# Performance work log

Hardware: AMD Instinct MI355X
Metric: run time of the kernel (lower is better)

The kernel has to match this reference:

```python
import jax, jax.numpy as jnp
import numpy as np

FACTOR = 1.0

def _dct_matrix():
    n = 8
    D = np.zeros((n * n, n * n), dtype=np.float32)
    for u in range(n):
        for v in range(n):
            au = 1.0 / np.sqrt(2.0) if u == 0 else 1.0
            av = 1.0 / np.sqrt(2.0) if v == 0 else 1.0
            alpha = au * av * 0.25
            for x in range(n):
                for y in range(n):
                    D[u * n + v, x * n + y] = alpha * np.cos((2 * x + 1) * u * np.pi / 16) * np.cos((2 * y + 1) * v * np.pi / 16)
    return D

def _y_quant_table():
    t = np.array([[16, 11, 10, 16, 24, 40, 51, 61], [12, 12, 14, 19, 26, 58, 60, 55],
                  [14, 13, 16, 24, 40, 57, 69, 56], [14, 17, 22, 29, 51, 87, 80, 62],
                  [18, 22, 37, 56, 68, 109, 103, 77], [24, 35, 55, 64, 81, 104, 113, 92],
                  [49, 64, 78, 87, 103, 121, 120, 101], [72, 92, 95, 98, 112, 100, 103, 99]],
                 dtype=np.float32).T
    return t

def _c_quant_table():
    t = np.full((8, 8), 99, dtype=np.float32)
    t[:4, :4] = np.array([[17, 18, 24, 47], [18, 21, 26, 66], [24, 26, 56, 99], [47, 66, 99, 99]],
                          dtype=np.float32).T
    return t

_D = jnp.asarray(_dct_matrix())          # [64,64]
_QT = jnp.stack([jnp.asarray(_y_quant_table()),
                 jnp.asarray(_c_quant_table()),
                 jnp.asarray(_c_quant_table())], axis=0) * FACTOR  # [3,8,8]

def setup_inputs() -> dict:
    key = jax.random.key(0)
    image = jax.random.uniform(key, (32, 3, 512, 512), dtype=jnp.float32)
    return {"image": image}

def _diffjpeg(image):
    x = jnp.clip(image, 0.0, 1.0)
    B, C, H, W = x.shape  # H, W multiples of 8 -> no padding branch
    r, g, b = x[:, 0], x[:, 1], x[:, 2]
    y = 0.299 * r + 0.587 * g + 0.114 * b
    cb = (b - y) * 0.564 + 0.5
    cr = (r - y) * 0.713 + 0.5
    ycbcr = jnp.stack([y, cb, cr], axis=1)  # [B,3,H,W]
    # blockify into 8x8 tiles
    nh, nw = H // 8, W // 8
    blocks = ycbcr.reshape(B, C, nh, 8, nw, 8).transpose(0, 1, 2, 4, 3, 5)  # [B,C,nh,nw,8,8]
    flat = blocks.reshape(-1, 64) * 255.0 - 128.0
    dct = flat @ _D.T                      # matmul(D, flat.T).T
    dctb = dct.reshape(B, C, nh, nw, 8, 8)
    qte = _QT[None, :, None, None, :, :]   # [1,3,1,1,8,8]
    q = dctb / qte
    q = q + jax.lax.stop_gradient(jnp.round(q) - q)  # STE rounding
    deq = q * qte
    idct = deq.reshape(-1, 64) @ _D        # matmul(D.T, x.T).T
    idct = (idct + 128.0) / 255.0
    img = idct.reshape(B, C, nh, nw, 8, 8).transpose(0, 1, 2, 4, 3, 5).reshape(B, C, H, W)
    yy, ycb, ycr = img[:, 0], img[:, 1] - 0.5, img[:, 2] - 0.5
    rr = yy + 1.403 * ycr
    gg = yy - 0.714 * ycr - 0.344 * ycb
    bb = yy + 1.773 * ycb
    rgb = jnp.clip(jnp.stack([rr, gg, bb], axis=1), 0.0, 1.0)
    return jnp.clip(rgb, 0.0, 1.0)

def reference(image):
    return _diffjpeg(image)
```

## Files before the change

kernel.cpp:

```cpp
#include <hip/hip_runtime.h>

static constexpr float CM[8][8] = {
    { 0.353553391f,  0.353553391f,  0.353553391f,  0.353553391f,  0.353553391f,  0.353553391f,  0.353553391f,  0.353553391f},
    { 0.490392640f,  0.415734806f,  0.277785117f,  0.097545161f, -0.097545161f, -0.277785117f, -0.415734806f, -0.490392640f},
    { 0.461939766f,  0.191341716f, -0.191341716f, -0.461939766f, -0.461939766f, -0.191341716f,  0.191341716f,  0.461939766f},
    { 0.415734806f, -0.097545161f, -0.490392640f, -0.277785117f,  0.277785117f,  0.490392640f,  0.097545161f, -0.415734806f},
    { 0.353553391f, -0.353553391f, -0.353553391f,  0.353553391f,  0.353553391f, -0.353553391f, -0.353553391f,  0.353553391f},
    { 0.277785117f, -0.490392640f,  0.097545161f,  0.415734806f, -0.415734806f, -0.097545161f,  0.490392640f, -0.277785117f},
    { 0.191341716f, -0.461939766f,  0.461939766f, -0.191341716f, -0.191341716f,  0.461939766f, -0.461939766f,  0.191341716f},
    { 0.097545161f, -0.277785117f,  0.415734806f, -0.490392640f,  0.490392640f, -0.415734806f,  0.277785117f, -0.097545161f}
};

__device__ const float YQ[64] = {
    16.f, 11.f, 10.f, 16.f,  24.f,  40.f,  51.f,  61.f,
    12.f, 12.f, 14.f, 19.f,  26.f,  58.f,  60.f,  55.f,
    14.f, 13.f, 16.f, 24.f,  40.f,  57.f,  69.f,  56.f,
    14.f, 17.f, 22.f, 29.f,  51.f,  87.f,  80.f,  62.f,
    18.f, 22.f, 37.f, 56.f,  68.f, 109.f, 103.f,  77.f,
    24.f, 35.f, 55.f, 64.f,  81.f, 104.f, 113.f,  92.f,
    49.f, 64.f, 78.f, 87.f, 103.f, 121.f, 120.f, 101.f,
    72.f, 92.f, 95.f, 98.f, 112.f, 100.f, 103.f,  99.f
};

__device__ const float CQ[64] = {
    17.f, 18.f, 24.f, 47.f, 99.f, 99.f, 99.f, 99.f,
    18.f, 21.f, 26.f, 66.f, 99.f, 99.f, 99.f, 99.f,
    24.f, 26.f, 56.f, 99.f, 99.f, 99.f, 99.f, 99.f,
    47.f, 66.f, 99.f, 99.f, 99.f, 99.f, 99.f, 99.f,
    99.f, 99.f, 99.f, 99.f, 99.f, 99.f, 99.f, 99.f,
    99.f, 99.f, 99.f, 99.f, 99.f, 99.f, 99.f, 99.f,
    99.f, 99.f, 99.f, 99.f, 99.f, 99.f, 99.f, 99.f,
    99.f, 99.f, 99.f, 99.f, 99.f, 99.f, 99.f, 99.f
};

#define LDSW 68

__global__ __launch_bounds__(256, 6) void diffjpeg_kernel(const float* __restrict__ in,
                                                          float* __restrict__ out)
{
    __shared__ __align__(16) float pl[3][32][LDSW];

    const int t   = threadIdx.x;
    const int col = t & 63;
    const int br  = t >> 6;

    const int bid  = blockIdx.x;
    const int img  = bid >> 7;
    const int rem  = bid & 127;
    const int trow = rem >> 3;
    const int tcol = rem & 7;
    const size_t HW = (size_t)512 * 512;
    const size_t tbase = (size_t)img * 3 * HW + (size_t)(trow * 32) * 512 + (size_t)(tcol * 64);
    const float* __restrict__ pin  = in  + tbase;
    float* __restrict__       pout = out + tbase;

    {
        const float* cbase = pin + (size_t)(br * 8) * 512 + col;
        float rv[8], gv[8], bv[8];
        #pragma unroll
        for (int x = 0; x < 8; ++x) rv[x] = cbase[(size_t)x * 512];
        #pragma unroll
        for (int x = 0; x < 8; ++x) gv[x] = cbase[HW + (size_t)x * 512];
        #pragma unroll
        for (int x = 0; x < 8; ++x) bv[x] = cbase[2 * HW + (size_t)x * 512];

        float yv[8], cbv[8], crv[8];
        #pragma unroll
        for (int x = 0; x < 8; ++x) {
            const float r = fminf(fmaxf(rv[x], 0.f), 1.f);
            const float g = fminf(fmaxf(gv[x], 0.f), 1.f);
            const float b = fminf(fmaxf(bv[x], 0.f), 1.f);
            const float y  = 0.299f * r + 0.587f * g + 0.114f * b;
            yv[x]  = y * 255.f - 128.f;
            cbv[x] = ((b - y) * 0.564f + 0.5f) * 255.f - 128.f;
            crv[x] = ((r - y) * 0.713f + 0.5f) * 255.f - 128.f;
        }

        #pragma unroll
        for (int u = 0; u < 8; ++u) {
            float sy = 0.f, scb = 0.f, scr = 0.f;
            #pragma unroll
            for (int x = 0; x < 8; ++x) {
                sy  += CM[u][x] * yv[x];
                scb += CM[u][x] * cbv[x];
                scr += CM[u][x] * crv[x];
            }
            pl[0][br * 8 + u][col] = sy;
            pl[1][br * 8 + u][col] = scb;
            pl[2][br * 8 + u][col] = scr;
        }
    }
    __syncthreads();

    {
        const int bc  = t & 7;
        const int u   = (t >> 3) & 7;
        const int row = (t >> 6) * 8 + u;
        #pragma unroll
        for (int c = 0; c < 3; ++c) {
            float4* rp = (float4*)&pl[c][row][bc * 8];
            const float4 a0 = rp[0];
            const float4 a1 = rp[1];
            const float T[8] = {a0.x, a0.y, a0.z, a0.w, a1.x, a1.y, a1.z, a1.w};
            float Dq[8];
            #pragma unroll
            for (int v = 0; v < 8; ++v) {
                float s = 0.f;
                #pragma unroll
                for (int y = 0; y < 8; ++y) s += CM[v][y] * T[y];
                const float qt = (c == 0) ? YQ[v * 8 + u] : CQ[u * 8 + v];
                Dq[v] = rintf(s / qt) * qt;
            }
            float4 o0, o1;
            float* op = (float*)&o0;
            #pragma unroll
            for (int y = 0; y < 8; ++y) {
                float s = 0.f;
                #pragma unroll
                for (int v = 0; v < 8; ++v) s += Dq[v] * CM[v][y];
                if (y < 4) op[y] = s; else ((float*)&o1)[y - 4] = s;
            }
            rp[0] = o0;
            rp[1] = o1;
        }
    }
    __syncthreads();

    {
        float Xy[8], Xcb[8], Xcr[8];
        #pragma unroll
        for (int u = 0; u < 8; ++u) {
            Xy[u]  = pl[0][br * 8 + u][col];
            Xcb[u] = pl[1][br * 8 + u][col];
            Xcr[u] = pl[2][br * 8 + u][col];
        }
        float* obase = pout + (size_t)(br * 8) * 512 + col;
        constexpr float inv255 = 1.0f / 255.0f;
        #pragma unroll
        for (int x = 0; x < 8; ++x) {
            float sy = 0.f, scb = 0.f, scr = 0.f;
            #pragma unroll
            for (int u = 0; u < 8; ++u) {
                sy  += CM[u][x] * Xy[u];
                scb += CM[u][x] * Xcb[u];
                scr += CM[u][x] * Xcr[u];
            }
            const float yy = (sy  + 128.f) * inv255;
            const float cb = (scb + 128.f) * inv255 - 0.5f;
            const float cr = (scr + 128.f) * inv255 - 0.5f;
            const float rr = yy + 1.403f * cr;
            const float gg = yy - 0.714f * cr - 0.344f * cb;
            const float bb = yy + 1.773f * cb;
            obase[(size_t)x * 512]          = fminf(fmaxf(rr, 0.f), 1.f);
            obase[HW + (size_t)x * 512]     = fminf(fmaxf(gg, 0.f), 1.f);
            obase[2 * HW + (size_t)x * 512] = fminf(fmaxf(bb, 0.f), 1.f);
        }
    }
}

extern "C" void kernel_launch(void* const* d_in, const int* in_sizes, int n_in,
                              void* d_out, int out_size, void* d_ws, size_t ws_size,
                              hipStream_t stream) {
    const float* in = (const float*)d_in[0];
    float* out = (float*)d_out;
    const int B = in_sizes[0] / (3 * 512 * 512);
    const int grid = B * 128;
    diffjpeg_kernel<<<grid, 256, 0, stream>>>(in, out);
}
```

Before: 42.08 us.

## Use butterfly DCT, wave-local LDS fences, folded color constants, nontemporal stores

```diff
diff --git a/kernel.cpp b/kernel.cpp
--- a/kernel.cpp
+++ b/kernel.cpp
@@ -1,28 +1,25 @@
 #include <hip/hip_runtime.h>
 
-static constexpr float CM[8][8] = {
-    { 0.353553391f,  0.353553391f,  0.353553391f,  0.353553391f,  0.353553391f,  0.353553391f,  0.353553391f,  0.353553391f},
-    { 0.490392640f,  0.415734806f,  0.277785117f,  0.097545161f, -0.097545161f, -0.277785117f, -0.415734806f, -0.490392640f},
-    { 0.461939766f,  0.191341716f, -0.191341716f, -0.461939766f, -0.461939766f, -0.191341716f,  0.191341716f,  0.461939766f},
-    { 0.415734806f, -0.097545161f, -0.490392640f, -0.277785117f,  0.277785117f,  0.490392640f,  0.097545161f, -0.415734806f},
-    { 0.353553391f, -0.353553391f, -0.353553391f,  0.353553391f,  0.353553391f, -0.353553391f, -0.353553391f,  0.353553391f},
-    { 0.277785117f, -0.490392640f,  0.097545161f,  0.415734806f, -0.415734806f, -0.097545161f,  0.490392640f, -0.277785117f},
-    { 0.191341716f, -0.461939766f,  0.461939766f, -0.191341716f, -0.191341716f,  0.461939766f, -0.461939766f,  0.191341716f},
-    { 0.097545161f, -0.277785117f,  0.415734806f, -0.490392640f,  0.490392640f, -0.415734806f,  0.277785117f, -0.097545161f}
+#define K4 0.353553391f
+#define K1 0.490392640f
+#define K3 0.415734806f
+#define K5 0.277785117f
+#define K7 0.097545161f
+#define K2 0.461939766f
+#define K6 0.191341716f
+
+__device__ __align__(16) const float YQT[64] = {
+    16.f, 12.f, 14.f, 14.f,  18.f,  24.f,  49.f,  72.f,
+    11.f, 12.f, 13.f, 17.f,  22.f,  35.f,  64.f,  92.f,
+    10.f, 14.f, 16.f, 22.f,  37.f,  55.f,  78.f,  95.f,
+    16.f, 19.f, 24.f, 29.f,  56.f,  64.f,  87.f,  98.f,
+    24.f, 26.f, 40.f, 51.f,  68.f,  81.f, 103.f, 112.f,
+    40.f, 58.f, 57.f, 87.f, 109.f, 104.f, 121.f, 100.f,
+    51.f, 60.f, 69.f, 80.f, 103.f, 113.f, 120.f, 103.f,
+    61.f, 55.f, 56.f, 62.f,  77.f,  92.f, 101.f,  99.f
 };
 
-__device__ const float YQ[64] = {
-    16.f, 11.f, 10.f, 16.f,  24.f,  40.f,  51.f,  61.f,
-    12.f, 12.f, 14.f, 19.f,  26.f,  58.f,  60.f,  55.f,
-    14.f, 13.f, 16.f, 24.f,  40.f,  57.f,  69.f,  56.f,
-    14.f, 17.f, 22.f, 29.f,  51.f,  87.f,  80.f,  62.f,
-    18.f, 22.f, 37.f, 56.f,  68.f, 109.f, 103.f,  77.f,
-    24.f, 35.f, 55.f, 64.f,  81.f, 104.f, 113.f,  92.f,
-    49.f, 64.f, 78.f, 87.f, 103.f, 121.f, 120.f, 101.f,
-    72.f, 92.f, 95.f, 98.f, 112.f, 100.f, 103.f,  99.f
-};
-
-__device__ const float CQ[64] = {
+__device__ __align__(16) const float CQ[64] = {
     17.f, 18.f, 24.f, 47.f, 99.f, 99.f, 99.f, 99.f,
     18.f, 21.f, 26.f, 66.f, 99.f, 99.f, 99.f, 99.f,
     24.f, 26.f, 56.f, 99.f, 99.f, 99.f, 99.f, 99.f,
@@ -33,6 +30,41 @@
     99.f, 99.f, 99.f, 99.f, 99.f, 99.f, 99.f, 99.f
 };
 
+__device__ __forceinline__ void dct8(const float x[8], float X[8]) {
+    const float a0 = x[0] + x[7], a1 = x[1] + x[6], a2 = x[2] + x[5], a3 = x[3] + x[4];
+    const float d0 = x[0] - x[7], d1 = x[1] - x[6], d2 = x[2] - x[5], d3 = x[3] - x[4];
+    const float e0 = a0 + a3, e1 = a1 + a2, f0 = a0 - a3, f1 = a1 - a2;
+    X[0] = K4 * (e0 + e1);
+    X[4] = K4 * (e0 - e1);
+    X[2] = K2 * f0 + K6 * f1;
+    X[6] = K6 * f0 - K2 * f1;
+    X[1] = K1 * d0 + K3 * d1 + K5 * d2 + K7 * d3;
+    X[3] = K3 * d0 - K7 * d1 - K1 * d2 - K5 * d3;
+    X[5] = K5 * d0 - K1 * d1 + K7 * d2 + K3 * d3;
+    X[7] = K7 * d0 - K5 * d1 + K3 * d2 - K1 * d3;
+}
+
+__device__ __forceinline__ void idct8(const float X[8], float x[8]) {
+    const float g0 = K4 * (X[0] + X[4]);
+    const float g1 = K4 * (X[0] - X[4]);
+    const float E0 = g0 + K2 * X[2] + K6 * X[6];
+    const float E1 = g1 + K6 * X[2] - K2 * X[6];
+    const float E2 = g1 - K6 * X[2] + K2 * X[6];
+    const float E3 = g0 - K2 * X[2] - K6 * X[6];
+    const float O0 = K1 * X[1] + K3 * X[3] + K5 * X[5] + K7 * X[7];
+    const float O1 = K3 * X[1] - K7 * X[3] - K1 * X[5] - K5 * X[7];
+    const float O2 = K5 * X[1] - K1 * X[3] + K7 * X[5] + K3 * X[7];
+    const float O3 = K7 * X[1] - K5 * X[3] + K3 * X[5] - K1 * X[7];
+    x[0] = E0 + O0;  x[7] = E0 - O0;
+    x[1] = E1 + O1;  x[6] = E1 - O1;
+    x[2] = E2 + O2;  x[5] = E2 - O2;
+    x[3] = E3 + O3;  x[4] = E3 - O3;
+}
+
+__device__ __forceinline__ void wave_lds_fence() {
+    asm volatile("s_waitcnt lgkmcnt(0)" ::: "memory");
+}
+
 #define LDSW 68
 
 __global__ __launch_bounds__(256, 6) void diffjpeg_kernel(const float* __restrict__ in,
@@ -40,9 +72,10 @@
 {
     __shared__ __align__(16) float pl[3][32][LDSW];
 
-    const int t   = threadIdx.x;
-    const int col = t & 63;
-    const int br  = t >> 6;
+    const int t  = threadIdx.x;
+    const int l  = t & 63;
+    const int wv = t >> 6;
+    const int r0 = wv * 8;
 
     const int bid  = blockIdx.x;
     const int img  = bid >> 7;
@@ -50,19 +83,19 @@
     const int trow = rem >> 3;
     const int tcol = rem & 7;
     const size_t HW = (size_t)512 * 512;
-    const size_t tbase = (size_t)img * 3 * HW + (size_t)(trow * 32) * 512 + (size_t)(tcol * 64);
-    const float* __restrict__ pin  = in  + tbase;
-    float* __restrict__       pout = out + tbase;
+    const size_t sbase = (size_t)img * 3 * HW + (size_t)(trow * 32 + wv * 8) * 512 + (size_t)(tcol * 64);
+    const float* __restrict__ pin  = in  + sbase;
+    float* __restrict__       pout = out + sbase;
 
     {
-        const float* cbase = pin + (size_t)(br * 8) * 512 + col;
+        const float* cb = pin + l;
         float rv[8], gv[8], bv[8];
         #pragma unroll
-        for (int x = 0; x < 8; ++x) rv[x] = cbase[(size_t)x * 512];
+        for (int x = 0; x < 8; ++x) rv[x] = cb[(size_t)x * 512];
         #pragma unroll
-        for (int x = 0; x < 8; ++x) gv[x] = cbase[HW + (size_t)x * 512];
+        for (int x = 0; x < 8; ++x) gv[x] = cb[HW + (size_t)x * 512];
         #pragma unroll
-        for (int x = 0; x < 8; ++x) bv[x] = cbase[2 * HW + (size_t)x * 512];
+        for (int x = 0; x < 8; ++x) bv[x] = cb[2 * HW + (size_t)x * 512];
 
         float yv[8], cbv[8], crv[8];
         #pragma unroll
@@ -70,90 +103,85 @@
             const float r = fminf(fmaxf(rv[x], 0.f), 1.f);
             const float g = fminf(fmaxf(gv[x], 0.f), 1.f);
             const float b = fminf(fmaxf(bv[x], 0.f), 1.f);
-            const float y  = 0.299f * r + 0.587f * g + 0.114f * b;
-            yv[x]  = y * 255.f - 128.f;
-            cbv[x] = ((b - y) * 0.564f + 0.5f) * 255.f - 128.f;
-            crv[x] = ((r - y) * 0.713f + 0.5f) * 255.f - 128.f;
+            const float Y = fmaf(76.245f, r, fmaf(149.685f, g, 29.07f * b));
+            yv[x]  = Y - 128.f;
+            cbv[x] = fmaf(0.564f, fmaf(255.f, b, -Y), -0.5f);
+            crv[x] = fmaf(0.713f, fmaf(255.f, r, -Y), -0.5f);
         }
 
+        float X0[8], X1[8], X2[8];
+        dct8(yv,  X0);
+        dct8(cbv, X1);
+        dct8(crv, X2);
         #pragma unroll
         for (int u = 0; u < 8; ++u) {
-            float sy = 0.f, scb = 0.f, scr = 0.f;
-            #pragma unroll
-            for (int x = 0; x < 8; ++x) {
-                sy  += CM[u][x] * yv[x];
-                scb += CM[u][x] * cbv[x];
-                scr += CM[u][x] * crv[x];
-            }
-            pl[0][br * 8 + u][col] = sy;
-            pl[1][br * 8 + u][col] = scb;
-            pl[2][br * 8 + u][col] = scr;
+            pl[0][r0 + u][l] = X0[u];
+            pl[1][r0 + u][l] = X1[u];
+            pl[2][r0 + u][l] = X2[u];
         }
     }
-    __syncthreads();
+    wave_lds_fence();
 
     {
-        const int bc  = t & 7;
-        const int u   = (t >> 3) & 7;
-        const int row = (t >> 6) * 8 + u;
+        const int b8 = (l >> 3) * 8;
+        const int rr = l & 7;
+
+        const float4* yq4 = (const float4*)&YQT[rr * 8];
+        const float4* cq4 = (const float4*)&CQ[rr * 8];
+        const float4 yqa = yq4[0], yqb = yq4[1];
+        const float4 cqa = cq4[0], cqb = cq4[1];
+        const float yq[8] = {yqa.x, yqa.y, yqa.z, yqa.w, yqb.x, yqb.y, yqb.z, yqb.w};
+        const float cq[8] = {cqa.x, cqa.y, cqa.z, cqa.w, cqb.x, cqb.y, cqb.z, cqb.w};
+
         #pragma unroll
         for (int c = 0; c < 3; ++c) {
-            float4* rp = (float4*)&pl[c][row][bc * 8];
+            float4* rp = (float4*)&pl[c][r0 + rr][b8];
             const float4 a0 = rp[0];
             const float4 a1 = rp[1];
             const float T[8] = {a0.x, a0.y, a0.z, a0.w, a1.x, a1.y, a1.z, a1.w};
+            float S[8];
+            dct8(T, S);
             float Dq[8];
             #pragma unroll
             for (int v = 0; v < 8; ++v) {
-                float s = 0.f;
-                #pragma unroll
-                for (int y = 0; y < 8; ++y) s += CM[v][y] * T[y];
-                const float qt = (c == 0) ? YQ[v * 8 + u] : CQ[u * 8 + v];
-                Dq[v] = rintf(s / qt) * qt;
+                const float qt = (c == 0) ? yq[v] : cq[v];
+                Dq[v] = rintf(S[v] / qt) * qt;
             }
-            float4 o0, o1;
-            float* op = (float*)&o0;
-            #pragma unroll
-            for (int y = 0; y < 8; ++y) {
-                float s = 0.f;
-                #pragma unroll
-                for (int v = 0; v < 8; ++v) s += Dq[v] * CM[v][y];
-                if (y < 4) op[y] = s; else ((float*)&o1)[y - 4] = s;
-            }
-            rp[0] = o0;
-            rp[1] = o1;
+            float o[8];
+            idct8(Dq, o);
+            rp[0] = make_float4(o[0], o[1], o[2], o[3]);
+            rp[1] = make_float4(o[4], o[5], o[6], o[7]);
         }
     }
-    __syncthreads();
+    wave_lds_fence();
 
     {
         float Xy[8], Xcb[8], Xcr[8];
         #pragma unroll
         for (int u = 0; u < 8; ++u) {
-            Xy[u]  = pl[0][br * 8 + u][col];
-            Xcb[u] = pl[1][br * 8 + u][col];
-            Xcr[u] = pl[2][br * 8 + u][col];
+            Xy[u]  = pl[0][r0 + u][l];
+            Xcb[u] = pl[1][r0 + u][l];
+            Xcr[u] = pl[2][r0 + u][l];
         }
-        float* obase = pout + (size_t)(br * 8) * 512 + col;
+        float sy[8], scb[8], scr[8];
+        idct8(Xy,  sy);
+        idct8(Xcb, scb);
+        idct8(Xcr, scr);
+
+        float* ob = pout + l;
         constexpr float inv255 = 1.0f / 255.0f;
+        constexpr float Kr = 0.504711754f;
+        constexpr float Kg = 0.499886280f;
+        constexpr float Kb = 0.505437240f;
         #pragma unroll
         for (int x = 0; x < 8; ++x) {
-            float sy = 0.f, scb = 0.f, scr = 0.f;
-            #pragma unroll
-            for (int u = 0; u < 8; ++u) {
-                sy  += CM[u][x] * Xy[u];
-                scb += CM[u][x] * Xcb[u];
-                scr += CM[u][x] * Xcr[u];
-            }
-            const float yy = (sy  + 128.f) * inv255;
-            const float cb = (scb + 128.f) * inv255 - 0.5f;
-            const float cr = (scr + 128.f) * inv255 - 0.5f;
-            const float rr = yy + 1.403f * cr;
-            const float gg = yy - 0.714f * cr - 0.344f * cb;
-            const float bb = yy + 1.773f * cb;
-            obase[(size_t)x * 512]          = fminf(fmaxf(rr, 0.f), 1.f);
-            obase[HW + (size_t)x * 512]     = fminf(fmaxf(gg, 0.f), 1.f);
-            obase[2 * HW + (size_t)x * 512] = fminf(fmaxf(bb, 0.f), 1.f);
+            const float rr = fmaf(inv255, fmaf(1.403f, scr[x], sy[x]), Kr);
+            const float tg = fmaf(-0.714f, scr[x], fmaf(-0.344f, scb[x], sy[x]));
+            const float gg = fmaf(inv255, tg, Kg);
+            const float bb = fmaf(inv255, fmaf(1.773f, scb[x], sy[x]), Kb);
+            __builtin_nontemporal_store(fminf(fmaxf(rr, 0.f), 1.f), ob + (size_t)x * 512);
+            __builtin_nontemporal_store(fminf(fmaxf(gg, 0.f), 1.f), ob + HW + (size_t)x * 512);
+            __builtin_nontemporal_store(fminf(fmaxf(bb, 0.f), 1.f), ob + 2 * HW + (size_t)x * 512);
         }
     }
 }
```

Result: faster. 37.38 us (-11.2%).
